# Kernel optimization log

Measured on AMD Instinct MI355X. Metric: run time of the kernel, lower is better.

Reference implementation:

```python
import jax, jax.numpy as jnp
import numpy as np

N = 50000      # nodes
E = 1600000    # edges
DIN = 512      # input feature dim
H = 128        # hidden dim
DOUT = 8       # classes
EPS = 1e-5     # BatchNorm eps


def setup_inputs() -> dict:
    key = jax.random.key(0)
    ks = jax.random.split(key, 12)
    x = jax.random.normal(ks[0], (N, DIN), dtype=jnp.float32)
    edge_index = jax.random.randint(ks[1], (2, E), 0, N)
    # Glorot-ish linear weights per GCNConv, zero bias (PyG default resets bias to 0)
    W1 = jax.random.normal(ks[2], (DIN, H), jnp.float32) / np.float32(np.sqrt(DIN))
    b1 = jnp.zeros((H,), jnp.float32)
    W2 = jax.random.normal(ks[3], (H, H), jnp.float32) / np.float32(np.sqrt(H))
    b2 = jnp.zeros((H,), jnp.float32)
    W3 = jax.random.normal(ks[4], (H, DOUT), jnp.float32) / np.float32(np.sqrt(H))
    b3 = jnp.zeros((DOUT,), jnp.float32)
    g1 = jnp.ones((H,), jnp.float32)
    beta1 = jnp.zeros((H,), jnp.float32)
    g2 = jnp.ones((H,), jnp.float32)
    beta2 = jnp.zeros((H,), jnp.float32)
    return {"x": x, "edge_index": edge_index, "W1": W1, "b1": b1, "W2": W2,
            "b2": b2, "W3": W3, "b3": b3, "g1": g1, "beta1": beta1,
            "g2": g2, "beta2": beta2}


def _gcn_conv(h, W, b, src, dst, n):
    # PyG GCNConv: linear, add self-loops, sym-normalized scatter-add, + bias
    h = h @ W                                   # [n, out]
    loops = jnp.arange(n)
    s = jnp.concatenate([src, loops])           # [E+n]
    d = jnp.concatenate([dst, loops])
    deg = jax.ops.segment_sum(jnp.ones(s.shape, h.dtype), d, num_segments=n)
    dinv = jnp.where(deg > 0, jax.lax.rsqrt(deg), jnp.zeros((), h.dtype))
    norm = dinv[s] * dinv[d]                    # [E+n]
    out = jax.ops.segment_sum(h[s] * norm[:, None], d, num_segments=n)
    return out + b


def _bn(x, g, b):
    # BatchNorm1d forward with batch statistics (biased variance, as in torch training)
    mu = x.mean(axis=0)
    var = x.var(axis=0)
    return (x - mu) * jax.lax.rsqrt(var + EPS) * g + b


def reference(x, edge_index, W1, b1, W2, b2, W3, b3, g1, beta1, g2, beta2):
    src, dst = edge_index[0], edge_index[1]
    n = x.shape[0]
    h = _gcn_conv(x, W1, b1, src, dst, n)
    h = jax.nn.relu(_bn(h, g1, beta1))          # dropout inert at inference
    h = _gcn_conv(h, W2, b2, src, dst, n)
    h = jax.nn.relu(_bn(h, g2, beta2))
    h = _gcn_conv(h, W3, b3, src, dst, n)
    return jax.nn.log_softmax(h, axis=1)
```

## Files before the change

### kernel.cpp

```cpp
#include <hip/hip_runtime.h>
#include <math.h>

#define NN 50000
#define NE 1600000
#define DIN 512
#define HH 128
#define EPSBN 1e-5f
#define NB 782
#define PAD 16
#define CAPE 4096
#define CHUNK 6144
#define NBLK ((NE + CHUNK - 1) / CHUNK)

typedef __attribute__((ext_vector_type(8))) short bf16x8;
typedef __attribute__((ext_vector_type(4))) float f32x4;

__device__ __forceinline__ unsigned short f2bf(float f) {
    unsigned u = __builtin_bit_cast(unsigned, f);
    u += 0x7FFFu + ((u >> 16) & 1u);
    return (unsigned short)(u >> 16);
}
__device__ __forceinline__ unsigned packbf(float a, float b) {
    return (unsigned)f2bf(a) | ((unsigned)f2bf(b) << 16);
}
__device__ __forceinline__ float bf2f(unsigned short v) {
    return __builtin_bit_cast(float, (unsigned)v << 16);
}

__global__ void k_zero(int* __restrict__ bcnt, float* __restrict__ st) {
    int i = blockIdx.x * 256 + threadIdx.x;
    if (i < NB * PAD) bcnt[i] = 0;
    if (i < 512) st[i] = 0.0f;
}

__global__ __launch_bounds__(256) void k_hist(const int* __restrict__ dst,
                                              int* __restrict__ bcnt) {
    __shared__ int h[1024];
    int t = threadIdx.x;
    for (int i = t; i < 1024; i += 256) h[i] = 0;
    __syncthreads();
    int eb = blockIdx.x * CHUNK;
    int cnt = NE - eb;
    if (cnt > CHUNK) cnt = CHUNK;
    for (int i = t; i < cnt; i += 256) atomicAdd(&h[dst[eb + i] >> 6], 1);
    __syncthreads();
    for (int b = t; b < NB; b += 256) {
        int c = h[b];
        if (c) atomicAdd(&bcnt[b << 4], c);
    }
}

__global__ __launch_bounds__(1024) void k_bscan(int* __restrict__ bcnt,
                                                int* __restrict__ bbase,
                                                int* __restrict__ rowptr) {
    __shared__ int ps[1024];
    int t = threadIdx.x;
    int v = (t < NB) ? bcnt[t << 4] : 0;
    ps[t] = v;
    __syncthreads();
    for (int off = 1; off < 1024; off <<= 1) {
        int u = (t >= off) ? ps[t - off] : 0;
        __syncthreads();
        ps[t] += u;
        __syncthreads();
    }
    int ex = ps[t] - v;
    bbase[t] = ex;
    if (t < NB) bcnt[t << 4] = ex;
    if (t == 0) rowptr[NN] = NE;
}

__global__ __launch_bounds__(256) void k_part(const int* __restrict__ src,
                                              const int* __restrict__ dst,
                                              int* __restrict__ bcursor,
                                              unsigned* __restrict__ packed) {
    __shared__ unsigned stage[CHUNK];
    __shared__ unsigned stage2[CHUNK];
    __shared__ int hist[1024];
    __shared__ int prefix[1024];
    __shared__ int baseg[1024];
    __shared__ int ps[256];
    int t = threadIdx.x;
    int eb = blockIdx.x * CHUNK;
    int cnt = NE - eb;
    if (cnt > CHUNK) cnt = CHUNK;

    for (int i = t; i < 1024; i += 256) hist[i] = 0;
    __syncthreads();
    for (int i = t; i < cnt; i += 256) {
        int e = eb + i;
        unsigned s = (unsigned)src[e];
        unsigned d = (unsigned)dst[e];
        unsigned b = d >> 6;
        stage[i] = (b << 22) | ((d & 63u) << 16) | s;
        atomicAdd(&hist[b], 1);
    }
    __syncthreads();
    int b0 = t * 4;
    int h0 = hist[b0], h1 = hist[b0 + 1], h2 = hist[b0 + 2], h3 = hist[b0 + 3];
    int tot = h0 + h1 + h2 + h3;
    ps[t] = tot;
    __syncthreads();
    for (int off = 1; off < 256; off <<= 1) {
        int u = (t >= off) ? ps[t - off] : 0;
        __syncthreads();
        ps[t] += u;
        __syncthreads();
    }
    int ex = ps[t] - tot;
    prefix[b0] = ex;
    prefix[b0 + 1] = ex + h0;
    prefix[b0 + 2] = ex + h0 + h1;
    prefix[b0 + 3] = ex + h0 + h1 + h2;
    __syncthreads();
    for (int b = t; b < 1024; b += 256) {
        int c = hist[b];
        if (c > 0 && b < NB) baseg[b] = atomicAdd(&bcursor[b << 4], c);
        hist[b] = prefix[b];
    }
    __syncthreads();
    for (int i = t; i < cnt; i += 256) {
        unsigned pk = stage[i];
        int p = atomicAdd(&hist[pk >> 22], 1);
        stage2[p] = pk;
    }
    __syncthreads();
    for (int i = t; i < cnt; i += 256) {
        unsigned pk = stage2[i];
        unsigned b = pk >> 22;
        packed[baseg[b] + (i - prefix[b])] = pk;
    }
}

__global__ __launch_bounds__(256) void k_bfinal(const unsigned* __restrict__ packed,
                                                const int* __restrict__ bbase,
                                                int* __restrict__ csr_src,
                                                int* __restrict__ rowptr,
                                                float* __restrict__ dinv) {
    __shared__ unsigned pk[CAPE];
    __shared__ int outsrc[CAPE];
    __shared__ int hcnt[64], hoff[64], hcur[64];
    int b = blockIdx.x;
    int base = bbase[b];
    int cnt = bbase[b + 1] - base;
    if (cnt > CAPE) cnt = CAPE;
    int t = threadIdx.x;
    for (int i = t; i < cnt; i += 256) pk[i] = packed[base + i];
    if (t < 64) hcnt[t] = 0;
    __syncthreads();
    for (int i = t; i < cnt; i += 256) atomicAdd(&hcnt[(pk[i] >> 16) & 63u], 1);
    __syncthreads();
    if (t == 0) {
        int run = 0;
        for (int i = 0; i < 64; ++i) { hoff[i] = run; hcur[i] = run; run += hcnt[i]; }
    }
    __syncthreads();
    if (t < 64) {
        int node = b * 64 + t;
        if (node < NN) {
            rowptr[node] = base + hoff[t];
            dinv[node] = rsqrtf((float)(hcnt[t] + 1));
        }
    }
    for (int i = t; i < cnt; i += 256) {
        int lpos = atomicAdd(&hcur[(pk[i] >> 16) & 63u], 1);
        outsrc[lpos] = (int)(pk[i] & 0xFFFFu);
    }
    __syncthreads();
    for (int i = t; i < cnt; i += 256) csr_src[base + i] = outsrc[i];
}

#define WGT_BLKS ((NN + 255) / 256)
__global__ void k_prep(const int* __restrict__ rowptr, const int* __restrict__ csr_src,
                       const float* __restrict__ dinv, unsigned* __restrict__ epk,
                       const float* __restrict__ W1, const float* __restrict__ W2,
                       unsigned short* __restrict__ W1t, unsigned short* __restrict__ W2t) {
    if (blockIdx.x < WGT_BLKS) {
        int g = blockIdx.x * 256 + threadIdx.x;
        if (g >= NN) return;
        float dd = dinv[g];
        int end = rowptr[g + 1];
        for (int e = rowptr[g]; e < end; ++e) {
            int s = csr_src[e];
            epk[e] = ((unsigned)f2bf(dinv[s] * dd) << 16) | (unsigned)s;
        }
    } else {
        int i = (blockIdx.x - WGT_BLKS) * 256 + threadIdx.x;
        if (i < 512 * 128) {
            int k = i >> 7, n = i & 127;
            W1t[n * 512 + k] = f2bf(W1[i]);
        }
        if (i < 128 * 128) {
            int k = i >> 7, n = i & 127;
            W2t[n * 128 + k] = f2bf(W2[i]);
        }
    }
}

__global__ __launch_bounds__(256) void k_gemm1(const float* __restrict__ A,
                                               const unsigned short* __restrict__ Wt,
                                               unsigned short* __restrict__ Cb,
                                               int M, int K) {
    __shared__ unsigned short As[64][72];
    __shared__ unsigned short Bs[128][72];
    const int tid = threadIdx.x;
    const int m0 = blockIdx.x * 64;
    const int w = tid >> 6;
    const int lane = tid & 63;
    const int cr = lane & 15;
    const int half = lane >> 4;
    const int arow = tid >> 2;
    const int akseg = (tid & 3) << 4;
    const int brow = tid >> 1;
    const int bkseg = (tid & 1) << 5;

    f32x4 acc[8];
#pragma unroll
    for (int n = 0; n < 8; ++n) acc[n] = (f32x4){0.f, 0.f, 0.f, 0.f};

    for (int kc = 0; kc < K; kc += 64) {
        float4 va[4];
        int gm = m0 + arow;
        if (gm < M) {
            const float* ap = A + (size_t)gm * K + kc + akseg;
#pragma unroll
            for (int i = 0; i < 4; ++i) va[i] = ((const float4*)ap)[i];
        } else {
#pragma unroll
            for (int i = 0; i < 4; ++i) va[i] = make_float4(0.f, 0.f, 0.f, 0.f);
        }
        uint4 q0, q1;
        q0.x = packbf(va[0].x, va[0].y); q0.y = packbf(va[0].z, va[0].w);
        q0.z = packbf(va[1].x, va[1].y); q0.w = packbf(va[1].z, va[1].w);
        q1.x = packbf(va[2].x, va[2].y); q1.y = packbf(va[2].z, va[2].w);
        q1.z = packbf(va[3].x, va[3].y); q1.w = packbf(va[3].z, va[3].w);
        *(uint4*)(&As[arow][akseg]) = q0;
        *(uint4*)(&As[arow][akseg + 8]) = q1;
        {
            const unsigned short* wp = Wt + (size_t)brow * K + kc + bkseg;
            uint4* bp = (uint4*)(&Bs[brow][bkseg]);
#pragma unroll
            for (int i = 0; i < 4; ++i) bp[i] = ((const uint4*)wp)[i];
        }
        __syncthreads();
        const int wrow = w << 4;
#pragma unroll
        for (int ks = 0; ks < 2; ++ks) {
            bf16x8 af = *(const bf16x8*)(&As[wrow + cr][ks * 32 + half * 8]);
#pragma unroll
            for (int n = 0; n < 8; ++n) {
                bf16x8 bfr = *(const bf16x8*)(&Bs[n * 16 + cr][ks * 32 + half * 8]);
                acc[n] = __builtin_amdgcn_mfma_f32_16x16x32_bf16(af, bfr, acc[n], 0, 0, 0);
            }
        }
        __syncthreads();
    }
#pragma unroll
    for (int n = 0; n < 8; ++n) {
        int col = n * 16 + cr;
        size_t cbase = (size_t)(col >> 5) * NN * 32 + (col & 31);
#pragma unroll
        for (int reg = 0; reg < 4; ++reg) {
            int gr = m0 + (w << 4) + half * 4 + reg;
            if (gr < M) Cb[cbase + (size_t)gr * 32] = f2bf(acc[n][reg]);
        }
    }
}

__global__ __launch_bounds__(256) void k_gemm2(const unsigned short* __restrict__ A,
                                               const unsigned short* __restrict__ Wt,
                                               const float* __restrict__ st,
                                               const float* __restrict__ gam,
                                               const float* __restrict__ beta,
                                               unsigned short* __restrict__ Cb,
                                               int M) {
    __shared__ unsigned short As[64][72];
    __shared__ unsigned short Bs[128][72];
    __shared__ float scs[128], shs[128];
    const int tid = threadIdx.x;
    const int m0 = blockIdx.x * 64;
    const int w = tid >> 6;
    const int lane = tid & 63;
    const int cr = lane & 15;
    const int half = lane >> 4;
    const int arow = tid >> 2;
    const int akseg = (tid & 3) << 4;
    const int brow = tid >> 1;
    const int bkseg = (tid & 1) << 5;

    if (tid < 128) {
        const float invn = 1.0f / (float)NN;
        float mu = st[tid] * invn;
        float var = fmaf(-mu, mu, st[tid + 128] * invn);
        float s = gam[tid] * rsqrtf(var + EPSBN);
        scs[tid] = s;
        shs[tid] = fmaf(-mu, s, beta[tid]);
    }

    f32x4 acc[8];
#pragma unroll
    for (int n = 0; n < 8; ++n) acc[n] = (f32x4){0.f, 0.f, 0.f, 0.f};

    for (int kc = 0; kc < 128; kc += 64) {
        uint4 q0 = {0, 0, 0, 0}, q1 = {0, 0, 0, 0};
        int gm = m0 + arow;
        if (gm < M) {
            const uint4* ap = (const uint4*)(A + (size_t)gm * 128 + kc + akseg);
            q0 = ap[0];
            q1 = ap[1];
        }
        if (kc == 0) __syncthreads();
        int kb = kc + akseg;
        unsigned qq[8] = {q0.x, q0.y, q0.z, q0.w, q1.x, q1.y, q1.z, q1.w};
#pragma unroll
        for (int j = 0; j < 8; ++j) {
            int k = kb + j * 2;
            float lo = fmaxf(fmaf(bf2f((unsigned short)(qq[j] & 0xFFFFu)), scs[k], shs[k]), 0.f);
            float hi = fmaxf(fmaf(bf2f((unsigned short)(qq[j] >> 16)), scs[k + 1], shs[k + 1]), 0.f);
            qq[j] = packbf(lo, hi);
        }
        *(uint4*)(&As[arow][akseg])     = make_uint4(qq[0], qq[1], qq[2], qq[3]);
        *(uint4*)(&As[arow][akseg + 8]) = make_uint4(qq[4], qq[5], qq[6], qq[7]);
        {
            const unsigned short* wp = Wt + (size_t)brow * 128 + kc + bkseg;
            uint4* bp = (uint4*)(&Bs[brow][bkseg]);
#pragma unroll
            for (int i = 0; i < 4; ++i) bp[i] = ((const uint4*)wp)[i];
        }
        __syncthreads();
        const int wrow = w << 4;
#pragma unroll
        for (int ks = 0; ks < 2; ++ks) {
            bf16x8 af = *(const bf16x8*)(&As[wrow + cr][ks * 32 + half * 8]);
#pragma unroll
            for (int n = 0; n < 8; ++n) {
                bf16x8 bfr = *(const bf16x8*)(&Bs[n * 16 + cr][ks * 32 + half * 8]);
                acc[n] = __builtin_amdgcn_mfma_f32_16x16x32_bf16(af, bfr, acc[n], 0, 0, 0);
            }
        }
        __syncthreads();
    }
#pragma unroll
    for (int n = 0; n < 8; ++n) {
        int col = n * 16 + cr;
        size_t cbase = (size_t)(col >> 5) * NN * 32 + (col & 31);
#pragma unroll
        for (int reg = 0; reg < 4; ++reg) {
            int gr = m0 + (w << 4) + half * 4 + reg;
            if (gr < M) Cb[cbase + (size_t)gr * 32] = f2bf(acc[n][reg]);
        }
    }
}

__global__ __launch_bounds__(256) void k_gather128b(const unsigned short* __restrict__ tb,
                                                    const int* __restrict__ rowptr,
                                                    const unsigned* __restrict__ epk,
                                                    const float* __restrict__ dinv,
                                                    const float* __restrict__ bias,
                                                    unsigned short* __restrict__ h,
                                                    int chunk) {
    int g = (blockIdx.x * 256 + threadIdx.x) >> 3;
    if (g >= NN) return;
    int lane8 = threadIdx.x & 7;
    int co = lane8 * 4;
    const unsigned short* tab = tb + (size_t)chunk * NN * 32;
    int beg = rowptr[g], end = rowptr[g + 1];
    float dd = dinv[g];
    ushort4 sv = *(const ushort4*)(tab + (size_t)g * 32 + co);
    float4 bv = *(const float4*)(bias + chunk * 32 + co);
    float wself = dd * dd;
    float ax = fmaf(bf2f(sv.x), wself, bv.x);
    float ay = fmaf(bf2f(sv.y), wself, bv.y);
    float az = fmaf(bf2f(sv.z), wself, bv.z);
    float aw = fmaf(bf2f(sv.w), wself, bv.w);
    for (int base = beg; base < end; base += 8) {
        int idx = base + lane8;
        unsigned pe = (idx < end) ? epk[idx] : 0u;
#pragma unroll
        for (int j = 0; j < 8; ++j) {
            unsigned pj = __shfl(pe, j, 8);
            float w = bf2f((unsigned short)(pj >> 16));
            int s = (int)(pj & 0xFFFFu);
            ushort4 v = *(const ushort4*)(tab + (size_t)s * 32 + co);
            ax = fmaf(bf2f(v.x), w, ax);
            ay = fmaf(bf2f(v.y), w, ay);
            az = fmaf(bf2f(v.z), w, az);
            aw = fmaf(bf2f(v.w), w, aw);
        }
    }
    ushort4 o;
    o.x = f2bf(ax); o.y = f2bf(ay); o.z = f2bf(az); o.w = f2bf(aw);
    *(ushort4*)(h + (size_t)g * 128 + chunk * 32 + co) = o;
}

__global__ __launch_bounds__(256) void k_bnstats(const unsigned short* __restrict__ h,
                                                 float* __restrict__ sums,
                                                 float* __restrict__ sumsq) {
    int c4 = (threadIdx.x & 31) * 4;
    int rg = threadIdx.x >> 5;
    float s1x = 0, s1y = 0, s1z = 0, s1w = 0;
    float s2x = 0, s2y = 0, s2z = 0, s2w = 0;
    for (int r = blockIdx.x * 8 + rg; r < NN; r += gridDim.x * 8) {
        ushort4 u = *(const ushort4*)(h + (size_t)r * 128 + c4);
        float vx = bf2f(u.x), vy = bf2f(u.y), vz = bf2f(u.z), vw = bf2f(u.w);
        s1x += vx; s1y += vy; s1z += vz; s1w += vw;
        s2x = fmaf(vx, vx, s2x);
        s2y = fmaf(vy, vy, s2y);
        s2z = fmaf(vz, vz, s2z);
        s2w = fmaf(vw, vw, s2w);
    }
    __shared__ float l1[256][4];
    __shared__ float l2[256][4];
    l1[threadIdx.x][0] = s1x; l1[threadIdx.x][1] = s1y;
    l1[threadIdx.x][2] = s1z; l1[threadIdx.x][3] = s1w;
    l2[threadIdx.x][0] = s2x; l2[threadIdx.x][1] = s2y;
    l2[threadIdx.x][2] = s2z; l2[threadIdx.x][3] = s2w;
    __syncthreads();
    if (rg == 0) {
        int lane = threadIdx.x & 31;
#pragma unroll
        for (int gg = 1; gg < 8; ++gg) {
            int o = gg * 32 + lane;
            s1x += l1[o][0]; s1y += l1[o][1]; s1z += l1[o][2]; s1w += l1[o][3];
            s2x += l2[o][0]; s2y += l2[o][1]; s2z += l2[o][2]; s2w += l2[o][3];
        }
        atomicAdd(&sums[c4 + 0], s1x);
        atomicAdd(&sums[c4 + 1], s1y);
        atomicAdd(&sums[c4 + 2], s1z);
        atomicAdd(&sums[c4 + 3], s1w);
        atomicAdd(&sumsq[c4 + 0], s2x);
        atomicAdd(&sumsq[c4 + 1], s2y);
        atomicAdd(&sumsq[c4 + 2], s2z);
        atomicAdd(&sumsq[c4 + 3], s2w);
    }
}

__global__ __launch_bounds__(256) void k_gemm8_bn(const unsigned short* __restrict__ A,
                                                  const float* __restrict__ W,
                                                  const float* __restrict__ st,
                                                  const float* __restrict__ gam,
                                                  const float* __restrict__ beta,
                                                  float* __restrict__ C, int M) {
    __shared__ float Ws[128 * 8];
    __shared__ float scs[128], shs[128];
    int tid = threadIdx.x;
    for (int i = tid; i < 128 * 8; i += 256) Ws[i] = W[i];
    if (tid < 128) {
        const float invn = 1.0f / (float)NN;
        float mu = st[tid] * invn;
        float var = fmaf(-mu, mu, st[tid + 128] * invn);
        float s = gam[tid] * rsqrtf(var + EPSBN);
        scs[tid] = s;
        shs[tid] = fmaf(-mu, s, beta[tid]);
    }
    __syncthreads();
    int m = blockIdx.x * 32 + (tid >> 3);
    int n = tid & 7;
    if (m >= M) return;
    const unsigned short* a = A + (size_t)m * 128;
    float s = 0.0f;
#pragma unroll
    for (int k = 0; k < 128; k += 8) {
        uint4 q = *(const uint4*)(a + k);
        unsigned qq[4] = {q.x, q.y, q.z, q.w};
#pragma unroll
        for (int j = 0; j < 4; ++j) {
            int kk = k + j * 2;
            float lo = fmaxf(fmaf(bf2f((unsigned short)(qq[j] & 0xFFFFu)), scs[kk], shs[kk]), 0.f);
            float hi = fmaxf(fmaf(bf2f((unsigned short)(qq[j] >> 16)), scs[kk + 1], shs[kk + 1]), 0.f);
            s = fmaf(lo, Ws[kk * 8 + n], s);
            s = fmaf(hi, Ws[(kk + 1) * 8 + n], s);
        }
    }
    C[(size_t)m * 8 + n] = s;
}

__global__ __launch_bounds__(256) void k_gather8_lsm(const float* __restrict__ t,
                                                     const int* __restrict__ rowptr,
                                                     const unsigned* __restrict__ epk,
                                                     const float* __restrict__ dinv,
                                                     const float* __restrict__ bias,
                                                     float* __restrict__ out) {
    int g = (blockIdx.x * 256 + threadIdx.x) >> 3;
    if (g >= NN) return;
    int c = threadIdx.x & 7;
    int beg = rowptr[g], end = rowptr[g + 1];
    float dd = dinv[g];
    float acc = fmaf(t[(size_t)g * 8 + c], dd * dd, bias[c]);
    for (int base = beg; base < end; base += 8) {
        int idx = base + c;
        unsigned pe = (idx < end) ? epk[idx] : 0u;
#pragma unroll
        for (int j = 0; j < 8; ++j) {
            unsigned pj = __shfl(pe, j, 8);
            float w = bf2f((unsigned short)(pj >> 16));
            int s = (int)(pj & 0xFFFFu);
            acc = fmaf(t[(size_t)s * 8 + c], w, acc);
        }
    }
    float mx = acc;
#pragma unroll
    for (int m = 1; m < 8; m <<= 1) mx = fmaxf(mx, __shfl_xor(mx, m, 8));
    float ex = expf(acc - mx);
    float se = ex;
#pragma unroll
    for (int m = 1; m < 8; m <<= 1) se += __shfl_xor(se, m, 8);
    out[(size_t)g * 8 + c] = acc - (logf(se) + mx);
}

extern "C" void kernel_launch(void* const* d_in, const int* in_sizes, int n_in,
                              void* d_out, int out_size, void* d_ws, size_t ws_size,
                              hipStream_t stream) {
    const float* x     = (const float*)d_in[0];
    const int*   eidx  = (const int*)d_in[1];
    const float* W1    = (const float*)d_in[2];
    const float* b1    = (const float*)d_in[3];
    const float* W2    = (const float*)d_in[4];
    const float* b2    = (const float*)d_in[5];
    const float* W3    = (const float*)d_in[6];
    const float* b3    = (const float*)d_in[7];
    const float* g1    = (const float*)d_in[8];
    const float* beta1 = (const float*)d_in[9];
    const float* g2    = (const float*)d_in[10];
    const float* beta2 = (const float*)d_in[11];
    float* out = (float*)d_out;

    const int* src = eidx;
    const int* dst = eidx + NE;

    char* ws = (char*)d_ws;
    int*   bcnt    = (int*)ws;            ws += 51200 * 4;
    int*   bbase   = (int*)ws;            ws += 2048 * 4;
    int*   rowptr  = (int*)ws;            ws += 51200 * 4;
    float* dinv    = (float*)ws;          ws += 51200 * 4;
    float* st      = (float*)ws;          ws += 512 * 4;
    int*   csr_src = (int*)ws;            ws += (size_t)NE * 4;
    unsigned* epk  = (unsigned*)ws;       ws += (size_t)NE * 4;
    unsigned short* W1t = (unsigned short*)ws;  ws += 128 * 512 * 2;
    unsigned short* W2t = (unsigned short*)ws;  ws += 128 * 128 * 2;
    unsigned short* Ab  = (unsigned short*)ws;  ws += (size_t)4 * NN * 32 * 2;
    unsigned short* Bf  = (unsigned short*)ws;  ws += (size_t)NN * 128 * 2;
    float* C       = (float*)ws;
    unsigned* packed = (unsigned*)Ab;

    k_zero<<<(NB * PAD + 255) / 256, 256, 0, stream>>>(bcnt, st);
    k_hist<<<NBLK, 256, 0, stream>>>(dst, bcnt);
    k_bscan<<<1, 1024, 0, stream>>>(bcnt, bbase, rowptr);
    k_part<<<NBLK, 256, 0, stream>>>(src, dst, bcnt, packed);
    k_bfinal<<<NB, 256, 0, stream>>>(packed, bbase, csr_src, rowptr, dinv);
    k_prep<<<WGT_BLKS + 256, 256, 0, stream>>>(rowptr, csr_src, dinv, epk, W1, W2, W1t, W2t);

    const int ggrid = (NN * 8 + 255) / 256;

    k_gemm1<<<(NN + 63) / 64, 256, 0, stream>>>(x, W1t, Ab, NN, DIN);
    for (int ch = 0; ch < 4; ++ch)
        k_gather128b<<<ggrid, 256, 0, stream>>>(Ab, rowptr, epk, dinv, b1, Bf, ch);
    k_bnstats<<<512, 256, 0, stream>>>(Bf, st, st + 128);

    k_gemm2<<<(NN + 63) / 64, 256, 0, stream>>>(Bf, W2t, st, g1, beta1, Ab, NN);
    for (int ch = 0; ch < 4; ++ch)
        k_gather128b<<<ggrid, 256, 0, stream>>>(Ab, rowptr, epk, dinv, b2, Bf, ch);
    k_bnstats<<<512, 256, 0, stream>>>(Bf, st + 256, st + 384);

    k_gemm8_bn<<<(NN + 31) / 32, 256, 0, stream>>>(Bf, W3, st + 256, g2, beta2, C, NN);
    k_gather8_lsm<<<(NN * 8 + 255) / 256, 256, 0, stream>>>(C, rowptr, epk, dinv, b3, out);
}
```

Baseline: 384.8 us.

## Parallelize edge-weight prep per edge and prefetch next edge batch in gathers

k_bfinal now writes the destination node into the upper bits of epk along with the source, which removes the csr_src buffer. k_prep can then compute the normalized edge weight with one thread per edge instead of one thread per node looping serially over its row, which was load-imbalanced. The gather kernels also prefetch the next batch of 8 packed edges before processing the current one, to hide load latency. Both changes depend on node ids fitting in 16 bits, as the existing packing already assumes.

```diff
diff --git a/kernel.cpp b/kernel.cpp
--- a/kernel.cpp
+++ b/kernel.cpp
@@ -134,11 +134,11 @@
 
 __global__ __launch_bounds__(256) void k_bfinal(const unsigned* __restrict__ packed,
                                                 const int* __restrict__ bbase,
-                                                int* __restrict__ csr_src,
+                                                unsigned* __restrict__ epk,
                                                 int* __restrict__ rowptr,
                                                 float* __restrict__ dinv) {
     __shared__ unsigned pk[CAPE];
-    __shared__ int outsrc[CAPE];
+    __shared__ unsigned outv[CAPE];
     __shared__ int hcnt[64], hoff[64], hcur[64];
     int b = blockIdx.x;
     int base = bbase[b];
@@ -163,29 +163,31 @@
         }
     }
     for (int i = t; i < cnt; i += 256) {
-        int lpos = atomicAdd(&hcur[(pk[i] >> 16) & 63u], 1);
-        outsrc[lpos] = (int)(pk[i] & 0xFFFFu);
-    }
-    __syncthreads();
-    for (int i = t; i < cnt; i += 256) csr_src[base + i] = outsrc[i];
-}
-
-#define WGT_BLKS ((NN + 255) / 256)
-__global__ void k_prep(const int* __restrict__ rowptr, const int* __restrict__ csr_src,
-                       const float* __restrict__ dinv, unsigned* __restrict__ epk,
+        unsigned v = pk[i] & 0x3FFFFFu;
+        int lpos = atomicAdd(&hcur[v >> 16], 1);
+        outv[lpos] = v;
+    }
+    __syncthreads();
+    const unsigned dbase = ((unsigned)(b * 64)) << 16;
+    for (int i = t; i < cnt; i += 256)
+        epk[base + i] = dbase + outv[i];
+}
+
+#define PREP_EBLKS ((NE + 255) / 256)
+__global__ void k_prep(const float* __restrict__ dinv, unsigned* __restrict__ epk,
                        const float* __restrict__ W1, const float* __restrict__ W2,
                        unsigned short* __restrict__ W1t, unsigned short* __restrict__ W2t) {
-    if (blockIdx.x < WGT_BLKS) {
-        int g = blockIdx.x * 256 + threadIdx.x;
-        if (g >= NN) return;
-        float dd = dinv[g];
-        int end = rowptr[g + 1];
-        for (int e = rowptr[g]; e < end; ++e) {
-            int s = csr_src[e];
-            epk[e] = ((unsigned)f2bf(dinv[s] * dd) << 16) | (unsigned)s;
+    int bid = blockIdx.x;
+    if (bid < PREP_EBLKS) {
+        int e = bid * 256 + threadIdx.x;
+        if (e < NE) {
+            unsigned pe = epk[e];
+            unsigned s = pe & 0xFFFFu;
+            unsigned d = pe >> 16;
+            epk[e] = ((unsigned)f2bf(dinv[s] * dinv[d]) << 16) | s;
         }
     } else {
-        int i = (blockIdx.x - WGT_BLKS) * 256 + threadIdx.x;
+        int i = (bid - PREP_EBLKS) * 256 + threadIdx.x;
         if (i < 512 * 128) {
             int k = i >> 7, n = i & 127;
             W1t[n * 512 + k] = f2bf(W1[i]);
@@ -373,9 +375,11 @@
     float ay = fmaf(bf2f(sv.y), wself, bv.y);
     float az = fmaf(bf2f(sv.z), wself, bv.z);
     float aw = fmaf(bf2f(sv.w), wself, bv.w);
+    int idx0 = beg + lane8;
+    unsigned pe = (idx0 < end) ? epk[idx0] : 0u;
     for (int base = beg; base < end; base += 8) {
-        int idx = base + lane8;
-        unsigned pe = (idx < end) ? epk[idx] : 0u;
+        int nidx = base + 8 + lane8;
+        unsigned pe_next = (nidx < end) ? epk[nidx] : 0u;
 #pragma unroll
         for (int j = 0; j < 8; ++j) {
             unsigned pj = __shfl(pe, j, 8);
@@ -387,6 +391,7 @@
             az = fmaf(bf2f(v.z), w, az);
             aw = fmaf(bf2f(v.w), w, aw);
         }
+        pe = pe_next;
     }
     ushort4 o;
     o.x = f2bf(ax); o.y = f2bf(ay); o.z = f2bf(az); o.w = f2bf(aw);
@@ -487,9 +492,11 @@
     int beg = rowptr[g], end = rowptr[g + 1];
     float dd = dinv[g];
     float acc = fmaf(t[(size_t)g * 8 + c], dd * dd, bias[c]);
+    int idx0 = beg + c;
+    unsigned pe = (idx0 < end) ? epk[idx0] : 0u;
     for (int base = beg; base < end; base += 8) {
-        int idx = base + c;
-        unsigned pe = (idx < end) ? epk[idx] : 0u;
+        int nidx = base + 8 + c;
+        unsigned pe_next = (nidx < end) ? epk[nidx] : 0u;
 #pragma unroll
         for (int j = 0; j < 8; ++j) {
             unsigned pj = __shfl(pe, j, 8);
@@ -497,6 +504,7 @@
             int s = (int)(pj & 0xFFFFu);
             acc = fmaf(t[(size_t)s * 8 + c], w, acc);
         }
+        pe = pe_next;
     }
     float mx = acc;
 #pragma unroll
@@ -534,7 +542,6 @@
     int*   rowptr  = (int*)ws;            ws += 51200 * 4;
     float* dinv    = (float*)ws;          ws += 51200 * 4;
     float* st      = (float*)ws;          ws += 512 * 4;
-    int*   csr_src = (int*)ws;            ws += (size_t)NE * 4;
     unsigned* epk  = (unsigned*)ws;       ws += (size_t)NE * 4;
     unsigned short* W1t = (unsigned short*)ws;  ws += 128 * 512 * 2;
     unsigned short* W2t = (unsigned short*)ws;  ws += 128 * 128 * 2;
@@ -547,8 +554,8 @@
     k_hist<<<NBLK, 256, 0, stream>>>(dst, bcnt);
     k_bscan<<<1, 1024, 0, stream>>>(bcnt, bbase, rowptr);
     k_part<<<NBLK, 256, 0, stream>>>(src, dst, bcnt, packed);
-    k_bfinal<<<NB, 256, 0, stream>>>(packed, bbase, csr_src, rowptr, dinv);
-    k_prep<<<WGT_BLKS + 256, 256, 0, stream>>>(rowptr, csr_src, dinv, epk, W1, W2, W1t, W2t);
+    k_bfinal<<<NB, 256, 0, stream>>>(packed, bbase, epk, rowptr, dinv);
+    k_prep<<<PREP_EBLKS + 256, 256, 0, stream>>>(dinv, epk, W1, W2, W1t, W2t);
 
     const int ggrid = (NN * 8 + 255) / 256;
 
```

After: 372.6 us. 1.03x faster.
